# Optimization experiments

Hardware: AMD Instinct MI355X
Metric: run time of the kernel (lower is better)

The kernel has to match this reference:

```python
import jax, jax.numpy as jnp
import numpy as np
from jax import lax

NPRE = 900        # num_proposal_pre (hardcoded in module)
NPOST = 64        # num_proposal init arg
MAXV = 8          # max vertices of intersection of two convex quads
NMS_THRESH = 0.85
BN_EPS = 1e-5


def boxes3d_to_bev(b):
    # b: (N,7) = (x,y,z,h,w,l,ry) -> BEV rotated box (x1,y1,x2,y2,ry) on x-z plane
    cu, cv = b[:, 0], b[:, 2]
    half_l, half_w = b[:, 5] * 0.5, b[:, 4] * 0.5
    return jnp.stack([cu - half_l, cv - half_w, cu + half_l, cv + half_w, b[:, 6]], axis=-1)


def rect_corners(bev):
    # bev: (N,5) -> (N,4,2) CCW corners of rotated rect
    cx = (bev[:, 0] + bev[:, 2]) * 0.5
    cy = (bev[:, 1] + bev[:, 3]) * 0.5
    hx = (bev[:, 2] - bev[:, 0]) * 0.5
    hy = (bev[:, 3] - bev[:, 1]) * 0.5
    c, s = jnp.cos(bev[:, 4]), jnp.sin(bev[:, 4])
    lx = jnp.stack([-hx, hx, hx, -hx], -1)   # (N,4)
    ly = jnp.stack([-hy, -hy, hy, hy], -1)
    X = cx[:, None] + c[:, None] * lx - s[:, None] * ly
    Y = cy[:, None] + s[:, None] * lx + c[:, None] * ly
    return jnp.stack([X, Y], -1)


def _clip(poly, cnt, a, b):
    # Sutherland-Hodgman clip of poly (MAXV,2) with cnt valid verts by half-plane
    # left of directed edge a->b (clip quad is CCW).
    n = b - a
    def side(p):
        return n[0] * (p[1] - a[1]) - n[1] * (p[0] - a[0])
    out = jnp.zeros_like(poly)
    ocnt = jnp.int32(0)
    for i in range(MAXV):
        valid = i < cnt
        cur = poly[i]
        nxt = poly[jnp.where(i + 1 < cnt, i + 1, 0)]
        dc, dn = side(cur), side(nxt)
        in_c, in_n = dc >= 0, dn >= 0
        e1 = valid & in_c
        out = jnp.where(e1, out.at[ocnt].set(cur), out)
        ocnt = ocnt + e1.astype(jnp.int32)
        e2 = valid & (in_c != in_n)
        denom = dc - dn
        t = dc / jnp.where(denom == 0, 1.0, denom)
        ip = cur + t * (nxt - cur)
        out = jnp.where(e2, out.at[ocnt].set(ip), out)
        ocnt = ocnt + e2.astype(jnp.int32)
    return out, ocnt


def _pair_inter(ca, cb):
    # intersection area of two convex quads given CCW corners (4,2)
    poly = jnp.concatenate([ca, jnp.zeros((MAXV - 4, 2), ca.dtype)], 0)
    cnt = jnp.int32(4)
    for k in range(4):
        poly, cnt = _clip(poly, cnt, cb[k], cb[(k + 1) % 4])
    s = jnp.float32(0.0)
    for i in range(MAXV):
        valid = (i < cnt) & (cnt >= 3)
        j = jnp.where(i + 1 < cnt, i + 1, 0)
        s = s + jnp.where(valid, poly[i, 0] * poly[j, 1] - poly[j, 0] * poly[i, 1], 0.0)
    return jnp.abs(s) * 0.5


def pairwise_iou(corners, areas):
    # row-blocked to keep memory small: lax.map over rows, vmap over cols
    def row(args):
        ci, ai = args
        inter = jax.vmap(lambda cj: _pair_inter(ci, cj))(corners)
        return inter / jnp.maximum(ai + areas - inter, 1e-8)
    return lax.map(row, (corners, areas))


def nms_keep(iou):
    N = iou.shape[0]
    idx = jnp.arange(N)
    def body(i, keep):
        sup = keep[i] & (iou[i] > NMS_THRESH) & (idx > i)
        return keep & (~sup)
    return lax.fori_loop(0, N, body, jnp.ones((N,), bool))


def _forward(search_xyz, search_feature, estimation_cla, template_box,
             W1, b1, gamma, beta, run_mean, run_var, W2, b2):
    B, N = search_xyz.shape[0], search_xyz.shape[1]
    # reg head: conv1d(256->128,k1) + BN(eval) + ReLU + dropout(eval=id) + conv1d(128->4,k1)
    h = jnp.einsum('oi,bin->bon', W1, search_feature) + b1[None, :, None]
    inv = gamma / jnp.sqrt(run_var + BN_EPS)
    h = h * inv[None, :, None] + (beta - run_mean * inv)[None, :, None]
    h = jax.nn.relu(h)
    offset = jnp.einsum('oi,bin->bon', W2, h) + b2[None, :, None]  # (B,4,N)
    offset = jnp.transpose(offset, (0, 2, 1))                       # (B,N,4)
    vote_xyz = search_xyz + offset[..., 0:3]
    tmpl = jnp.broadcast_to(template_box, (B, N, 7))
    proposals = jnp.concatenate([vote_xyz, tmpl[..., 3:6], offset[..., 3:4]], -1)  # (B,N,7)
    scores = jax.nn.sigmoid(estimation_cla[..., 0])  # (B,N)

    def per_batch(sc, pr):
        order = jnp.argsort(-sc)
        s = sc[order[:NPRE]]
        p = pr[order[:NPRE]]
        bev = boxes3d_to_bev(p)
        corners = rect_corners(bev)
        areas = (bev[:, 2] - bev[:, 0]) * (bev[:, 3] - bev[:, 1])
        iou = pairwise_iou(lax.stop_gradient(corners), lax.stop_gradient(areas))
        keep = nms_keep(iou)
        rank = jnp.cumsum(keep.astype(jnp.int32)) - 1
        tgt = jnp.where(keep & (rank < NPOST), rank, NPOST)  # NPOST = dummy slot
        out_b = jnp.zeros((NPOST + 1, 7), p.dtype).at[tgt].set(p)[:NPOST]
        out_s = jnp.zeros((NPOST + 1,), s.dtype).at[tgt].set(s)[:NPOST]
        return out_b, out_s

    ret_bbox3d, ret_scores = jax.vmap(per_batch)(scores, proposals)
    center_xyzs = ret_bbox3d[..., 0:3]
    prop_out = jnp.take(proposals, jnp.array([0, 1, 2, 6]), axis=-1)
    return ret_bbox3d, ret_scores, prop_out, center_xyzs


def setup_inputs():
    key = jax.random.key(0)
    ks = jax.random.split(key, 8)
    B, N, C, H = 8, 16384, 256, 128
    search_xyz = jax.random.normal(ks[0], (B, N, 3), jnp.float32) * 2.0
    search_feature = jax.random.normal(ks[1], (B, C, N), jnp.float32)
    estimation_cla = jax.random.normal(ks[2], (B, N, 1), jnp.float32)
    center = jax.random.normal(ks[3], (B, 1, 3), jnp.float32)
    dims = jax.random.uniform(ks[4], (B, 1, 3), jnp.float32, 1.0, 3.0)
    ry = jax.random.uniform(ks[5], (B, 1, 1), jnp.float32, -np.pi, np.pi)
    template_box = jnp.concatenate([center, dims, ry], -1)
    W1 = jax.random.normal(ks[6], (H, C), jnp.float32) * (1.0 / np.sqrt(C))
    b1 = jnp.zeros((H,), jnp.float32)
    gamma = jnp.ones((H,), jnp.float32)
    beta = jnp.zeros((H,), jnp.float32)
    run_mean = jnp.zeros((H,), jnp.float32)
    run_var = jnp.ones((H,), jnp.float32)
    W2 = jax.random.normal(ks[7], (4, H), jnp.float32) * (1.0 / np.sqrt(H))
    b2 = jnp.zeros((4,), jnp.float32)
    return dict(search_xyz=search_xyz, search_feature=search_feature,
                estimation_cla=estimation_cla, template_box=template_box,
                W1=W1, b1=b1, gamma=gamma, beta=beta,
                run_mean=run_mean, run_var=run_var, W2=W2, b2=b2)


def reference(search_xyz, search_feature, estimation_cla, template_box,
              W1, b1, gamma, beta, run_mean, run_var, W2, b2):
    return _forward(search_xyz, search_feature, estimation_cla, template_box,
                    W1, b1, gamma, beta, run_mean, run_var, W2, b2)
```

## Files before the change

### kernel.cpp

```cpp
#include <hip/hip_runtime.h>
#include <cmath>

#define NTOT 16384
#define NBATCH 8
#define NPRE 900
#define NPOST 64

__global__ __launch_bounds__(256) void mlp_kernel(
    const float* __restrict__ feat, const float* __restrict__ xyz,
    const float* __restrict__ W1, const float* __restrict__ b1,
    const float* __restrict__ gamma, const float* __restrict__ beta,
    const float* __restrict__ rmean, const float* __restrict__ rvar,
    const float* __restrict__ W2, const float* __restrict__ b2,
    float* __restrict__ prop) {
  __shared__ float As[64][128];
  __shared__ float Bs[64][128];
  const int b  = blockIdx.y;
  const int n0 = blockIdx.x * 128;
  const int tid = threadIdx.x;
  const int tr = tid >> 4, tc = tid & 15;
  const float* fb = feat + (size_t)b * 256 * NTOT;

  float acc[8][8];
#pragma unroll
  for (int r = 0; r < 8; ++r)
#pragma unroll
    for (int c = 0; c < 8; ++c) acc[r][c] = 0.f;

  for (int kt = 0; kt < 4; ++kt) {
    {
      const int m = tid & 127, qh = tid >> 7;
#pragma unroll
      for (int p = 0; p < 8; ++p) {
        const int q = qh + p * 2;
        const float4 w = *(const float4*)(W1 + (size_t)m * 256 + kt * 64 + q * 4);
        As[q * 4 + 0][m] = w.x; As[q * 4 + 1][m] = w.y;
        As[q * 4 + 2][m] = w.z; As[q * 4 + 3][m] = w.w;
      }
      const int qq = tid & 31, r0 = tid >> 5;
#pragma unroll
      for (int p = 0; p < 8; ++p) {
        const int k = r0 + p * 8;
        *(float4*)(&Bs[k][qq * 4]) =
            *(const float4*)(fb + (size_t)(kt * 64 + k) * NTOT + n0 + qq * 4);
      }
    }
    __syncthreads();
#pragma unroll 8
    for (int k = 0; k < 64; ++k) {
      float a[8], bb[8];
      *(float4*)&a[0]  = *(const float4*)&As[k][tr * 8];
      *(float4*)&a[4]  = *(const float4*)&As[k][tr * 8 + 4];
      *(float4*)&bb[0] = *(const float4*)&Bs[k][tc * 8];
      *(float4*)&bb[4] = *(const float4*)&Bs[k][tc * 8 + 4];
#pragma unroll
      for (int r = 0; r < 8; ++r)
#pragma unroll
        for (int c = 0; c < 8; ++c) acc[r][c] = fmaf(a[r], bb[c], acc[r][c]);
    }
    __syncthreads();
  }

  float po[4][8];
#pragma unroll
  for (int kk = 0; kk < 4; ++kk)
#pragma unroll
    for (int c = 0; c < 8; ++c) po[kk][c] = 0.f;
#pragma unroll
  for (int r = 0; r < 8; ++r) {
    const int row = tr * 8 + r;
    const float inv = gamma[row] / sqrtf(rvar[row] + 1e-5f);
    const float sh  = beta[row] - rmean[row] * inv;
    const float bb1 = b1[row];
    float w2v[4];
#pragma unroll
    for (int kk = 0; kk < 4; ++kk) w2v[kk] = W2[kk * 128 + row];
#pragma unroll
    for (int c = 0; c < 8; ++c) {
      float h = (acc[r][c] + bb1) * inv + sh;
      h = fmaxf(h, 0.f);
#pragma unroll
      for (int kk = 0; kk < 4; ++kk) po[kk][c] += w2v[kk] * h;
    }
  }
  float* po_lds = &As[0][0];
#pragma unroll
  for (int kk = 0; kk < 4; ++kk)
#pragma unroll
    for (int c = 0; c < 8; ++c)
      po_lds[((tr * 4 + kk) * 128) + tc * 8 + c] = po[kk][c];
  __syncthreads();
  float* off_lds = &Bs[0][0];
#pragma unroll
  for (int it = 0; it < 2; ++it) {
    const int idx = tid + it * 256;
    const int kk = idx >> 7, col = idx & 127;
    float sum = b2[kk];
#pragma unroll
    for (int t2 = 0; t2 < 16; ++t2) sum += po_lds[((t2 * 4 + kk) * 128) + col];
    off_lds[kk * 128 + col] = sum;
  }
  __syncthreads();
  if (tid < 128) {
    const int n = n0 + tid;
    const float* sx = xyz + ((size_t)b * NTOT + n) * 3;
    float4 o;
    o.x = sx[0] + off_lds[0 * 128 + tid];
    o.y = sx[1] + off_lds[1 * 128 + tid];
    o.z = sx[2] + off_lds[2 * 128 + tid];
    o.w = off_lds[3 * 128 + tid];
    *(float4*)(prop + ((size_t)b * NTOT + n) * 4) = o;
  }
}

__global__ __launch_bounds__(1024) void select_kernel(
    const float* __restrict__ cla, const float* __restrict__ prop,
    const float* __restrict__ tmpl, float* __restrict__ selbox,
    float* __restrict__ corners, float* __restrict__ areas) {
  __shared__ unsigned red[17];
  __shared__ int cnt_lds;
  __shared__ unsigned long long cand[1024];
  const int b = blockIdx.x, tid = threadIdx.x;
  unsigned key[16];
#pragma unroll
  for (int q = 0; q < 16; ++q) {
    const float x = cla[(size_t)b * NTOT + q * 1024 + tid];
    key[q] = __float_as_uint(1.0f / (1.0f + expf(-x)));
  }
  unsigned lo = 0u, hi = 0xFFFFFFFFu;
  while (hi - lo > 1u) {
    const unsigned mid = lo + ((hi - lo) >> 1);
    int c = 0;
#pragma unroll
    for (int q = 0; q < 16; ++q) c += (key[q] >= mid) ? 1 : 0;
#pragma unroll
    for (int off = 32; off > 0; off >>= 1) c += __shfl_down(c, off);
    __syncthreads();
    if ((tid & 63) == 0) red[tid >> 6] = (unsigned)c;
    __syncthreads();
    if (tid == 0) {
      unsigned s = 0;
      for (int w2 = 0; w2 < 16; ++w2) s += red[w2];
      red[16] = s;
    }
    __syncthreads();
    if (red[16] >= NPRE) lo = mid; else hi = mid;
  }
  const unsigned T = lo;
  if (tid == 0) cnt_lds = 0;
  cand[tid] = 0ull;
  __syncthreads();
#pragma unroll
  for (int q = 0; q < 16; ++q) {
    if (key[q] >= T) {
      const int pos = atomicAdd(&cnt_lds, 1);
      if (pos < 1024)
        cand[pos] = ((unsigned long long)key[q] << 32) |
                    (unsigned long long)(0xFFFFFFFFu - (unsigned)(q * 1024 + tid));
    }
  }
  __syncthreads();
  for (int k = 2; k <= 1024; k <<= 1) {
    for (int j = k >> 1; j > 0; j >>= 1) {
      if (tid < 512) {
        const int i = ((tid & ~(j - 1)) << 1) | (tid & (j - 1));
        const int l = i | j;
        const unsigned long long Pi = cand[i], Pl = cand[l];
        const bool asc = (i & k) == 0;
        if ((Pi < Pl) == asc) { cand[i] = Pl; cand[l] = Pi; }
      }
      __syncthreads();
    }
  }
  if (tid < NPRE) {
    const unsigned long long p = cand[tid];
    const int idx = (int)(0xFFFFFFFFu - (unsigned)(p & 0xFFFFFFFFull));
    const float score = __uint_as_float((unsigned)(p >> 32));
    const float4 pv = *(const float4*)(prop + ((size_t)b * NTOT + idx) * 4);
    const float d3 = tmpl[b * 7 + 3], d4 = tmpl[b * 7 + 4], d5 = tmpl[b * 7 + 5];
    const size_t o8 = ((size_t)b * NPRE + tid) * 8;
    selbox[o8 + 0] = pv.x; selbox[o8 + 1] = pv.y; selbox[o8 + 2] = pv.z;
    selbox[o8 + 3] = d3;   selbox[o8 + 4] = d4;   selbox[o8 + 5] = d5;
    selbox[o8 + 6] = pv.w; selbox[o8 + 7] = score;
    {
#pragma clang fp contract(off)
      const float cu = pv.x, cv = pv.z;
      const float hl = d5 * 0.5f, hw = d4 * 0.5f;
      const float x1 = cu - hl, y1 = cv - hw, x2 = cu + hl, y2 = cv + hw;
      const float cx = (x1 + x2) * 0.5f, cy = (y1 + y2) * 0.5f;
      const float hx = (x2 - x1) * 0.5f, hy = (y2 - y1) * 0.5f;
      const float cr = cosf(pv.w), sr = sinf(pv.w);
      const float lx[4] = {-hx, hx, hx, -hx};
      const float ly[4] = {-hy, -hy, hy, hy};
#pragma unroll
      for (int q = 0; q < 4; ++q) {
        corners[o8 + 2 * q]     = cx + cr * lx[q] - sr * ly[q];
        corners[o8 + 2 * q + 1] = cy + sr * lx[q] + cr * ly[q];
      }
      areas[(size_t)b * NPRE + tid] = (x2 - x1) * (y2 - y1);
    }
  }
}

__device__ __forceinline__ float polyclip_area(
    float s0x, float s0y, float s1x, float s1y,
    float s2x, float s2y, float s3x, float s3y,
    const float cjx[4], const float cjy[4], float2* pb, int tid) {
#pragma clang fp contract(off)
  float vx[8], vy[8], d[8];
  vx[0] = s0x; vy[0] = s0y; vx[1] = s1x; vy[1] = s1y;
  vx[2] = s2x; vy[2] = s2y; vx[3] = s3x; vy[3] = s3y;
#pragma unroll
  for (int v = 4; v < 8; ++v) { vx[v] = 0.f; vy[v] = 0.f; }
  int cnt = 4;
  int dst = 0;
#pragma unroll
  for (int e = 0; e < 4; ++e) {
    const float ax = cjx[e], ay = cjy[e];
    const float bx = cjx[(e + 1) & 3], by = cjy[(e + 1) & 3];
    const float nx = bx - ax, ny = by - ay;
    if (e > 0) {
      const int src = dst ^ 1;
#pragma unroll
      for (int v = 0; v < 8; ++v) {
        const float2 p = pb[(src * 8 + v) * 256 + tid];
        vx[v] = p.x; vy[v] = p.y;
      }
    }
#pragma unroll
    for (int v = 0; v < 8; ++v) d[v] = nx * (vy[v] - ay) - ny * (vx[v] - ax);
    int ocnt = 0;
#pragma unroll
    for (int v = 0; v < 8; ++v) {
      const bool valid = v < cnt;
      float nvx, nvy, dn;
      if (v == 7) {
        const bool big = cnt > 8;
        nvx = big ? vx[7] : vx[0]; nvy = big ? vy[7] : vy[0]; dn = big ? d[7] : d[0];
      } else {
        const bool wrap = (v + 1 >= cnt);
        nvx = wrap ? vx[0] : vx[v + 1];
        nvy = wrap ? vy[0] : vy[v + 1];
        dn  = wrap ? d[0]  : d[v + 1];
      }
      const float dc = d[v];
      const bool inc = dc >= 0.f, inn = dn >= 0.f;
      if (valid && inc) {
        if (ocnt < 8) pb[(dst * 8 + ocnt) * 256 + tid] = make_float2(vx[v], vy[v]);
        ++ocnt;
      }
      if (valid && (inc != inn)) {
        const float den = dc - dn;
        const float t = dc / ((den == 0.f) ? 1.0f : den);
        if (ocnt < 8)
          pb[(dst * 8 + ocnt) * 256 + tid] =
              make_float2(vx[v] + t * (nvx - vx[v]), vy[v] + t * (nvy - vy[v]));
        ++ocnt;
      }
    }
    cnt = ocnt;
    dst ^= 1;
  }
  const int fb2 = dst ^ 1;
#pragma unroll
  for (int v = 0; v < 8; ++v) {
    const float2 p = pb[(fb2 * 8 + v) * 256 + tid];
    vx[v] = p.x; vy[v] = p.y;
  }
  float s = 0.f;
#pragma unroll
  for (int v = 0; v < 8; ++v) {
    const bool valid = (v < cnt) && (cnt >= 3);
    float jx, jy;
    if (v == 7) {
      const bool big = cnt > 8;
      jx = big ? vx[7] : vx[0]; jy = big ? vy[7] : vy[0];
    } else {
      const bool wrap = (v + 1 >= cnt);
      jx = wrap ? vx[0] : vx[v + 1]; jy = wrap ? vy[0] : vy[v + 1];
    }
    s += valid ? (vx[v] * jy - jx * vy[v]) : 0.f;
  }
  return fabsf(s) * 0.5f;
}

__global__ __launch_bounds__(256) void iou_kernel(
    const float* __restrict__ corners, const float* __restrict__ areas,
    unsigned long long* __restrict__ sup) {
  __shared__ float2 pb[2 * 8 * 256];
  const int i = blockIdx.x, b = blockIdx.y, tid = threadIdx.x;
  const float* ci = corners + ((size_t)b * NPRE + i) * 8;
  const float ai = areas[(size_t)b * NPRE + i];
  const float s0x = ci[0], s0y = ci[1], s1x = ci[2], s1y = ci[3];
  const float s2x = ci[4], s2y = ci[5], s3x = ci[6], s3y = ci[7];
  for (int c = 0; c < 4; ++c) {
    const int j = c * 256 + tid;
    bool bit = false;
    if (j > i && j < NPRE) {
      const float* cj = corners + ((size_t)b * NPRE + j) * 8;
      float cjx[4], cjy[4];
#pragma unroll
      for (int q = 0; q < 4; ++q) { cjx[q] = cj[2 * q]; cjy[q] = cj[2 * q + 1]; }
      const float inter = polyclip_area(s0x, s0y, s1x, s1y, s2x, s2y, s3x, s3y,
                                        cjx, cjy, pb, tid);
      const float aj = areas[(size_t)b * NPRE + j];
      const float iou = inter / fmaxf(ai + aj - inter, 1e-8f);
      bit = iou > 0.85f;
    }
    const unsigned long long m = __ballot(bit);
    if ((tid & 63) == 0)
      sup[((size_t)b * NPRE + i) * 16 + (unsigned)(j >> 6)] = m;
  }
}

#define NMS_ROWS 904
__global__ __launch_bounds__(1024) void nms_kernel(
    const unsigned long long* __restrict__ sup,
    unsigned long long* __restrict__ keepw) {
  extern __shared__ unsigned long long rows[];
  const int b = blockIdx.x, tid = threadIdx.x;
  const unsigned long long* srow = sup + (size_t)b * NPRE * 16;
  for (int q = tid; q < NMS_ROWS * 16; q += 1024)
    rows[q] = (q < NPRE * 16) ? srow[q] : 0ull;
  __syncthreads();
  if (tid < 64) {
    const int lane = tid;
    const bool ld = lane < 16;
    unsigned long long kw = 0ull;
    if (lane < 14) kw = ~0ull;
    else if (lane == 14) kw = 0xFull;
    unsigned long long r0 = ld ? rows[0 * 16 + lane] : 0ull;
    unsigned long long r1 = ld ? rows[1 * 16 + lane] : 0ull;
    unsigned long long r2 = ld ? rows[2 * 16 + lane] : 0ull;
    unsigned long long r3 = ld ? rows[3 * 16 + lane] : 0ull;
#define NMS_STEP(ii, bufv)                                            \
    {                                                                 \
      const unsigned long long w = __shfl(kw, (ii) >> 6);             \
      if ((w >> ((ii) & 63)) & 1ull) kw &= ~(bufv);                   \
      bufv = ld ? rows[((ii) + 4) * 16 + lane] : 0ull;                \
    }
    for (int i = 0; i < NPRE; i += 4) {
      NMS_STEP(i + 0, r0)
      NMS_STEP(i + 1, r1)
      NMS_STEP(i + 2, r2)
      NMS_STEP(i + 3, r3)
    }
#undef NMS_STEP
    if (lane < 15) keepw[b * 16 + lane] = kw;
  }
}

__global__ __launch_bounds__(128) void out_kernel(
    const float* __restrict__ selbox,
    const unsigned long long* __restrict__ keepw, float* __restrict__ out) {
  const int b = blockIdx.x, t = threadIdx.x;
  float* retb = out + (size_t)b * (NPOST * 7);
  float* rets = out + (size_t)NBATCH * NPOST * 7 + (size_t)b * NPOST;
  float* cent = out + (size_t)NBATCH * NPOST * 7 + (size_t)NBATCH * NPOST +
                (size_t)NBATCH * NTOT * 4 + (size_t)b * (NPOST * 3);
  for (int q = t; q < NPOST * 7; q += 128) retb[q] = 0.f;
  if (t < NPOST) rets[t] = 0.f;
  for (int q = t; q < NPOST * 3; q += 128) cent[q] = 0.f;
  __syncthreads();
  if (t < 64) {
    const unsigned long long kws = (t < 15) ? keepw[b * 16 + t] : 0ull;
    const int pc = __popcll(kws);
    int inc = pc;
    for (int d2 = 1; d2 < 64; d2 <<= 1) {
      const int up = __shfl_up(inc, d2);
      if (t >= d2) inc += up;
    }
    const int ex = inc - pc;
    for (int it = 0; it < 15; ++it) {
      const int i = t + it * 64;
      const int w = (i >> 6) & 63;
      const unsigned long long kword = __shfl(kws, w);
      const int exw = __shfl(ex, w);
      if (i < NPRE) {
        const int bp = i & 63;
        if ((kword >> bp) & 1ull) {
          const int rank =
              exw + __popcll(kword & (((unsigned long long)1 << bp) - 1ull));
          if (rank < NPOST) {
            const float* sb = selbox + ((size_t)b * NPRE + i) * 8;
#pragma unroll
            for (int c = 0; c < 7; ++c) retb[rank * 7 + c] = sb[c];
            rets[rank] = sb[7];
            cent[rank * 3 + 0] = sb[0];
            cent[rank * 3 + 1] = sb[1];
            cent[rank * 3 + 2] = sb[2];
          }
        }
      }
    }
  }
}

extern "C" void kernel_launch(void* const* d_in, const int* in_sizes, int n_in,
                              void* d_out, int out_size, void* d_ws, size_t ws_size,
                              hipStream_t stream) {
  const float* xyz   = (const float*)d_in[0];
  const float* feat  = (const float*)d_in[1];
  const float* cla   = (const float*)d_in[2];
  const float* tmpl  = (const float*)d_in[3];
  const float* W1    = (const float*)d_in[4];
  const float* b1    = (const float*)d_in[5];
  const float* gamma = (const float*)d_in[6];
  const float* beta  = (const float*)d_in[7];
  const float* rmean = (const float*)d_in[8];
  const float* rvar  = (const float*)d_in[9];
  const float* W2    = (const float*)d_in[10];
  const float* b2    = (const float*)d_in[11];
  float* out  = (float*)d_out;
  float* prop = out + (size_t)NBATCH * NPOST * 7 + (size_t)NBATCH * NPOST;

  char* ws = (char*)d_ws;
  float* selbox  = (float*)(ws);
  float* corners = (float*)(ws + 230400);
  float* areas   = (float*)(ws + 460800);
  unsigned long long* sup   = (unsigned long long*)(ws + 489600);
  unsigned long long* keepw = (unsigned long long*)(ws + 1411200);

  mlp_kernel<<<dim3(NTOT / 128, NBATCH), 256, 0, stream>>>(
      feat, xyz, W1, b1, gamma, beta, rmean, rvar, W2, b2, prop);

  select_kernel<<<NBATCH, 1024, 0, stream>>>(cla, prop, tmpl, selbox, corners,
                                             areas);

  iou_kernel<<<dim3(NPRE, NBATCH), 256, 0, stream>>>(corners, areas, sup);

  (void)hipFuncSetAttribute((const void*)nms_kernel,
                            hipFuncAttributeMaxDynamicSharedMemorySize,
                            NMS_ROWS * 16 * (int)sizeof(unsigned long long));
  nms_kernel<<<NBATCH, 1024, NMS_ROWS * 16 * sizeof(unsigned long long),
               stream>>>(sup, keepw);

  out_kernel<<<NBATCH, 128, 0, stream>>>(selbox, keepw, out);
}
```

Measured before the change: 460.9 us.

## Add AABB prefilter to IoU, register-only polygon clip, and conflict-free GEMM LDS reads

Select now computes an axis-aligned bounding box for each selected box. The IoU kernel uses it to skip the exact polygon clip whenever the AABB overlap cannot reach the area needed for IoU above 0.85. The clip itself is rewritten to keep vertices in registers with predicated selects instead of a shared-memory ping-pong buffer. The MLP GEMM also changes the Bs column mapping (tc*4 and 64+tc*4) to reduce LDS bank conflicts. The register clip adds select work and register pressure, and the prefilter relies on the bound ov >= 0.45*(ai+aj) being conservative.

```diff
diff --git a/kernel.cpp b/kernel.cpp
--- a/kernel.cpp
+++ b/kernel.cpp
@@ -51,8 +51,8 @@
       float a[8], bb[8];
       *(float4*)&a[0]  = *(const float4*)&As[k][tr * 8];
       *(float4*)&a[4]  = *(const float4*)&As[k][tr * 8 + 4];
-      *(float4*)&bb[0] = *(const float4*)&Bs[k][tc * 8];
-      *(float4*)&bb[4] = *(const float4*)&Bs[k][tc * 8 + 4];
+      *(float4*)&bb[0] = *(const float4*)&Bs[k][tc * 4];
+      *(float4*)&bb[4] = *(const float4*)&Bs[k][64 + tc * 4];
 #pragma unroll
       for (int r = 0; r < 8; ++r)
 #pragma unroll
@@ -87,8 +87,10 @@
 #pragma unroll
   for (int kk = 0; kk < 4; ++kk)
 #pragma unroll
-    for (int c = 0; c < 8; ++c)
-      po_lds[((tr * 4 + kk) * 128) + tc * 8 + c] = po[kk][c];
+    for (int c = 0; c < 8; ++c) {
+      const int col = (c < 4) ? (tc * 4 + c) : (64 + tc * 4 + (c - 4));
+      po_lds[((tr * 4 + kk) * 128) + col] = po[kk][c];
+    }
   __syncthreads();
   float* off_lds = &Bs[0][0];
 #pragma unroll
@@ -116,7 +118,8 @@
 __global__ __launch_bounds__(1024) void select_kernel(
     const float* __restrict__ cla, const float* __restrict__ prop,
     const float* __restrict__ tmpl, float* __restrict__ selbox,
-    float* __restrict__ corners, float* __restrict__ areas) {
+    float* __restrict__ corners, float* __restrict__ areas,
+    float* __restrict__ aabb) {
   __shared__ unsigned red[17];
   __shared__ int cnt_lds;
   __shared__ unsigned long long cand[1024];
@@ -192,44 +195,46 @@
       const float cr = cosf(pv.w), sr = sinf(pv.w);
       const float lx[4] = {-hx, hx, hx, -hx};
       const float ly[4] = {-hy, -hy, hy, hy};
+      float bx0 = 1e30f, by0 = 1e30f, bx1 = -1e30f, by1 = -1e30f;
 #pragma unroll
       for (int q = 0; q < 4; ++q) {
-        corners[o8 + 2 * q]     = cx + cr * lx[q] - sr * ly[q];
-        corners[o8 + 2 * q + 1] = cy + sr * lx[q] + cr * ly[q];
+        const float X = cx + cr * lx[q] - sr * ly[q];
+        const float Y = cy + sr * lx[q] + cr * ly[q];
+        corners[o8 + 2 * q]     = X;
+        corners[o8 + 2 * q + 1] = Y;
+        bx0 = fminf(bx0, X); by0 = fminf(by0, Y);
+        bx1 = fmaxf(bx1, X); by1 = fmaxf(by1, Y);
       }
       areas[(size_t)b * NPRE + tid] = (x2 - x1) * (y2 - y1);
-    }
-  }
-}
-
-__device__ __forceinline__ float polyclip_area(
+      float4 bb; bb.x = bx0; bb.y = by0; bb.z = bx1; bb.w = by1;
+      *(float4*)(aabb + ((size_t)b * NPRE + tid) * 4) = bb;
+    }
+  }
+}
+
+__device__ __forceinline__ float polyclip_reg(
     float s0x, float s0y, float s1x, float s1y,
     float s2x, float s2y, float s3x, float s3y,
-    const float cjx[4], const float cjy[4], float2* pb, int tid) {
+    const float cjx[4], const float cjy[4]) {
 #pragma clang fp contract(off)
-  float vx[8], vy[8], d[8];
+  float vx[8], vy[8];
   vx[0] = s0x; vy[0] = s0y; vx[1] = s1x; vy[1] = s1y;
   vx[2] = s2x; vy[2] = s2y; vx[3] = s3x; vy[3] = s3y;
 #pragma unroll
   for (int v = 4; v < 8; ++v) { vx[v] = 0.f; vy[v] = 0.f; }
   int cnt = 4;
-  int dst = 0;
 #pragma unroll
   for (int e = 0; e < 4; ++e) {
     const float ax = cjx[e], ay = cjy[e];
     const float bx = cjx[(e + 1) & 3], by = cjy[(e + 1) & 3];
     const float nx = bx - ax, ny = by - ay;
-    if (e > 0) {
-      const int src = dst ^ 1;
-#pragma unroll
-      for (int v = 0; v < 8; ++v) {
-        const float2 p = pb[(src * 8 + v) * 256 + tid];
-        vx[v] = p.x; vy[v] = p.y;
-      }
-    }
+    float d[8];
 #pragma unroll
     for (int v = 0; v < 8; ++v) d[v] = nx * (vy[v] - ay) - ny * (vx[v] - ax);
-    int ocnt = 0;
+    float ox[8], oy[8];
+#pragma unroll
+    for (int v = 0; v < 8; ++v) { ox[v] = 0.f; oy[v] = 0.f; }
+    int oc = 0;
 #pragma unroll
     for (int v = 0; v < 8; ++v) {
       const bool valid = v < cnt;
@@ -245,27 +250,30 @@
       }
       const float dc = d[v];
       const bool inc = dc >= 0.f, inn = dn >= 0.f;
-      if (valid && inc) {
-        if (ocnt < 8) pb[(dst * 8 + ocnt) * 256 + tid] = make_float2(vx[v], vy[v]);
-        ++ocnt;
-      }
-      if (valid && (inc != inn)) {
-        const float den = dc - dn;
-        const float t = dc / ((den == 0.f) ? 1.0f : den);
-        if (ocnt < 8)
-          pb[(dst * 8 + ocnt) * 256 + tid] =
-              make_float2(vx[v] + t * (nvx - vx[v]), vy[v] + t * (nvy - vy[v]));
-        ++ocnt;
-      }
-    }
-    cnt = ocnt;
-    dst ^= 1;
-  }
-  const int fb2 = dst ^ 1;
-#pragma unroll
-  for (int v = 0; v < 8; ++v) {
-    const float2 p = pb[(fb2 * 8 + v) * 256 + tid];
-    vx[v] = p.x; vy[v] = p.y;
+      const bool e1 = valid && inc;
+#pragma unroll
+      for (int s2 = 0; s2 < 8; ++s2) {
+        const bool w_ = e1 && (oc == s2);
+        ox[s2] = w_ ? vx[v] : ox[s2];
+        oy[s2] = w_ ? vy[v] : oy[s2];
+      }
+      oc += e1 ? 1 : 0;
+      const bool e2 = valid && (inc != inn);
+      const float den = dc - dn;
+      const float t = dc / ((den == 0.f) ? 1.0f : den);
+      const float ipx = vx[v] + t * (nvx - vx[v]);
+      const float ipy = vy[v] + t * (nvy - vy[v]);
+#pragma unroll
+      for (int s2 = 0; s2 < 8; ++s2) {
+        const bool w_ = e2 && (oc == s2);
+        ox[s2] = w_ ? ipx : ox[s2];
+        oy[s2] = w_ ? ipy : oy[s2];
+      }
+      oc += e2 ? 1 : 0;
+    }
+#pragma unroll
+    for (int v = 0; v < 8; ++v) { vx[v] = ox[v]; vy[v] = oy[v]; }
+    cnt = oc;
   }
   float s = 0.f;
 #pragma unroll
@@ -286,26 +294,32 @@
 
 __global__ __launch_bounds__(256) void iou_kernel(
     const float* __restrict__ corners, const float* __restrict__ areas,
-    unsigned long long* __restrict__ sup) {
-  __shared__ float2 pb[2 * 8 * 256];
+    const float* __restrict__ aabb, unsigned long long* __restrict__ sup) {
   const int i = blockIdx.x, b = blockIdx.y, tid = threadIdx.x;
   const float* ci = corners + ((size_t)b * NPRE + i) * 8;
   const float ai = areas[(size_t)b * NPRE + i];
+  const float4 bi = *(const float4*)(aabb + ((size_t)b * NPRE + i) * 4);
   const float s0x = ci[0], s0y = ci[1], s1x = ci[2], s1y = ci[3];
   const float s2x = ci[4], s2y = ci[5], s3x = ci[6], s3y = ci[7];
   for (int c = 0; c < 4; ++c) {
     const int j = c * 256 + tid;
     bool bit = false;
     if (j > i && j < NPRE) {
-      const float* cj = corners + ((size_t)b * NPRE + j) * 8;
-      float cjx[4], cjy[4];
-#pragma unroll
-      for (int q = 0; q < 4; ++q) { cjx[q] = cj[2 * q]; cjy[q] = cj[2 * q + 1]; }
-      const float inter = polyclip_area(s0x, s0y, s1x, s1y, s2x, s2y, s3x, s3y,
-                                        cjx, cjy, pb, tid);
+      const float4 bj = *(const float4*)(aabb + ((size_t)b * NPRE + j) * 4);
       const float aj = areas[(size_t)b * NPRE + j];
-      const float iou = inter / fmaxf(ai + aj - inter, 1e-8f);
-      bit = iou > 0.85f;
+      const float ow = fminf(bi.z, bj.z) - fmaxf(bi.x, bj.x);
+      const float oh = fminf(bi.w, bj.w) - fmaxf(bi.y, bj.y);
+      const float ov = fmaxf(ow, 0.f) * fmaxf(oh, 0.f);
+      if (ov >= 0.45f * (ai + aj)) {
+        const float* cj = corners + ((size_t)b * NPRE + j) * 8;
+        float cjx[4], cjy[4];
+#pragma unroll
+        for (int q = 0; q < 4; ++q) { cjx[q] = cj[2 * q]; cjy[q] = cj[2 * q + 1]; }
+        const float inter = polyclip_reg(s0x, s0y, s1x, s1y, s2x, s2y,
+                                         s3x, s3y, cjx, cjy);
+        const float iou = inter / fmaxf(ai + aj - inter, 1e-8f);
+        bit = iou > 0.85f;
+      }
     }
     const unsigned long long m = __ballot(bit);
     if ((tid & 63) == 0)
@@ -418,16 +432,17 @@
   float* selbox  = (float*)(ws);
   float* corners = (float*)(ws + 230400);
   float* areas   = (float*)(ws + 460800);
-  unsigned long long* sup   = (unsigned long long*)(ws + 489600);
-  unsigned long long* keepw = (unsigned long long*)(ws + 1411200);
+  float* aabb    = (float*)(ws + 489600);
+  unsigned long long* sup   = (unsigned long long*)(ws + 604800);
+  unsigned long long* keepw = (unsigned long long*)(ws + 1526400);
 
   mlp_kernel<<<dim3(NTOT / 128, NBATCH), 256, 0, stream>>>(
       feat, xyz, W1, b1, gamma, beta, rmean, rvar, W2, b2, prop);
 
   select_kernel<<<NBATCH, 1024, 0, stream>>>(cla, prop, tmpl, selbox, corners,
-                                             areas);
-
-  iou_kernel<<<dim3(NPRE, NBATCH), 256, 0, stream>>>(corners, areas, sup);
+                                             areas, aabb);
+
+  iou_kernel<<<dim3(NPRE, NBATCH), 256, 0, stream>>>(corners, areas, aabb, sup);
 
   (void)hipFuncSetAttribute((const void*)nms_kernel,
                             hipFuncAttributeMaxDynamicSharedMemorySize,
```

New measurement: 526.1 us. 14.1% more time.
